# Performance work log

Measured on AMD Instinct MI355X. Metric: run time of the kernel, lower is better.

The kernel has to match this reference:

```python
import jax, jax.numpy as jnp
import numpy as np

B, T, D, H, HID = 1024, 128, 256, 512, 512
INITIAL_DT = 0.01
DT = 0.1  # uniform spacing of x_time -> n_tp == 1 every step (single Euler step)


def setup_inputs() -> dict:
    key = jax.random.key(0)
    ks = jax.random.split(key, 13)
    g = lambda k, shp, sc: (jax.random.normal(k, shp, dtype=jnp.float32) * sc)
    C = 2 * H + D  # GRU input: concat(h_mean, h_std, x)
    return {
        "x": jax.random.normal(ks[0], (B, T, D), dtype=jnp.float32),
        "x_time": jnp.arange(T, dtype=jnp.float32) * DT,
        # ODE func f(h): 2-layer tanh MLP
        "W1": g(ks[1], (H, HID), 1.0 / np.sqrt(H)),
        "b1": jnp.zeros((HID,), jnp.float32),
        "W2": g(ks[2], (HID, H), 1.0 / np.sqrt(HID)),
        "b2": jnp.zeros((H,), jnp.float32),
        # GRU unit (latent-ODE style): update gate, reset gate, new-state net
        "Wz": g(ks[3], (C, H), 1.0 / np.sqrt(C)),
        "bz": jnp.zeros((H,), jnp.float32),
        "Wr": g(ks[4], (C, H), 1.0 / np.sqrt(C)),
        "br": jnp.zeros((H,), jnp.float32),
        "Wn": g(ks[5], (C, 2 * H), 1.0 / np.sqrt(C)),
        "bn": jnp.zeros((2 * H,), jnp.float32),
    }


def reference(x, x_time, W1, b1, W2, b2, Wz, bz, Wr, br, Wn, bn):
    Bsz = x.shape[0]
    Hd = W1.shape[0]
    h0 = jnp.zeros((Bsz, Hd), x.dtype)
    std0 = jnp.zeros((Bsz, Hd), x.dtype)
    t0 = x_time[0] - INITIAL_DT

    def ode_f(h):  # dh/dt (autonomous MLP, as diffeq_solver ODE func)
        return jnp.tanh(h @ W1 + b1) @ W2 + b2

    def step(carry, inp):
        h, hstd, t_prev = carry
        xi, ti = inp
        dt = ti - t_prev
        # one Euler step of the ODE solver (n_tp<=1 for uniform x_time)
        h_ode = h + ode_f(h) * dt
        # GRU unit on (h_ode, hstd, xi)
        cat = jnp.concatenate([h_ode, hstd, xi], axis=-1)  # [B, 2H+D]
        z = jax.nn.sigmoid(cat @ Wz + bz)
        r = jax.nn.sigmoid(cat @ Wr + br)
        cat_r = jnp.concatenate([h_ode * r, hstd * r, xi], axis=-1)
        n_mean, n_std = jnp.split(cat_r @ Wn + bn, 2, axis=-1)
        n_std = jnp.abs(n_std)
        h_new = (1.0 - z) * n_mean + z * h_ode
        std_new = jnp.abs((1.0 - z) * n_std + z * hstd)
        return (h_new, std_new, ti), None

    xs = (jnp.swapaxes(x, 0, 1), x_time)  # [T,B,D], [T]
    (hT, stdT, _), _ = jax.lax.scan(step, (h0, std0, t0), xs)
    return hT, stdT
```

## Files before the change

kernel.cpp:

```cpp
#include <hip/hip_runtime.h>
#include <hip/hip_bf16.h>

#define B_SZ 1024
#define T_SZ 128
#define D_SZ 256
#define H_SZ 512
#define NBLK 256
#define NTHR 512
#define AUXS 0x1

typedef __attribute__((ext_vector_type(8))) short short8;
typedef __attribute__((ext_vector_type(4))) float f32x4;

__device__ inline f32x4 mfma16(short8 a, short8 b, f32x4 c) {
  return __builtin_amdgcn_mfma_f32_16x16x32_bf16(a, b, c, 0, 0, 0);
}

__device__ inline void st_bf16(__hip_bfloat16* p, float v) {
  union { __hip_bfloat16 b; unsigned short u; } cv;
  cv.b = __float2bfloat16(v);
  unsigned int vv = cv.u;
  asm volatile("global_store_short %0, %1, off" :: "v"(p), "v"(vv) : "memory");
}

template <int ROWS, int AUX>
__device__ __forceinline__ void stage512(const __hip_bfloat16* __restrict__ src,
                                         int strideElts, int row0, int k0,
                                         unsigned short* lds, int tid) {
  constexpr int CH = ROWS * 8;
#pragma unroll
  for (int it = 0; it * NTHR < CH; ++it) {
    int wbase = it * NTHR + ((tid >> 6) << 6);
    if (wbase < CH) {
      int chunk = it * NTHR + tid;
      int row = chunk >> 3, slot = chunk & 7;
      int ksrc = (slot ^ (row & 7)) << 3;
      const __hip_bfloat16* g = src + (size_t)(row0 + row) * strideElts + (k0 + ksrc);
      unsigned short* l = lds + (size_t)wbase * 8;
      __builtin_amdgcn_global_load_lds(
          (const __attribute__((address_space(1))) unsigned int*)g,
          (__attribute__((address_space(3))) unsigned int*)l, 16, 0, AUX);
    }
  }
}

__device__ __forceinline__ short8 ldfrag(const unsigned short* lds, int row, int slot) {
  int s = slot ^ (row & 7);
  return *(const short8*)(lds + row * 64 + s * 8);
}

template <int NT, int PB, typename SA, typename SB, typename CC>
__device__ __forceinline__ void gloop(int wv, SA sa, SB sb, CC cc) {
  sa(0, 0); sa(1, 1); sa(2, 2); sa(3, 3);
#pragma unroll 1
  for (int kt = 0; kt < NT; ++kt) {
    if (wv < 4) {
      if (kt == 0)           asm volatile("s_waitcnt vmcnt(3)" ::: "memory");
      else if (kt == 1)      asm volatile("s_waitcnt vmcnt(%0)" :: "i"(3 + PB) : "memory");
      else if (kt <= NT - 4) asm volatile("s_waitcnt vmcnt(%0)" :: "i"(3 + 2 * PB) : "memory");
      else if (kt == NT - 3) asm volatile("s_waitcnt vmcnt(%0)" :: "i"(2 + 2 * PB) : "memory");
      else if (kt == NT - 2) asm volatile("s_waitcnt vmcnt(%0)" :: "i"(1 + PB) : "memory");
      else                   asm volatile("s_waitcnt vmcnt(0)" ::: "memory");
    } else {
      if (kt <= NT - 3)      asm volatile("s_waitcnt vmcnt(%0)" :: "i"(2 * PB) : "memory");
      else if (kt == NT - 2) asm volatile("s_waitcnt vmcnt(%0)" :: "i"(PB) : "memory");
      else                   asm volatile("s_waitcnt vmcnt(0)" ::: "memory");
    }
    __builtin_amdgcn_s_barrier();
    __builtin_amdgcn_sched_barrier(0);
    if (kt + 3 < NT) sb(kt + 3, (kt + 3) & 3);
    if (kt + 4 < NT) sa(kt + 4, (kt + 4) % 5);
    cc(kt % 5, kt & 3);
  }
}

__device__ __forceinline__ void sbar_arrive(unsigned* scnt) {
  asm volatile("s_waitcnt vmcnt(0)" ::: "memory");
  __syncthreads();
  if (threadIdx.x == 0)
    __hip_atomic_fetch_add(scnt, 1u, __ATOMIC_RELAXED, __HIP_MEMORY_SCOPE_AGENT);
}
__device__ __forceinline__ void sbar_wait(unsigned* scnt, unsigned p) {
  if (threadIdx.x == 0) {
    while (__hip_atomic_load(scnt, __ATOMIC_RELAXED, __HIP_MEMORY_SCOPE_AGENT) < p * 8u)
      __builtin_amdgcn_s_sleep(1);
  }
  __syncthreads();
  __builtin_amdgcn_sched_barrier(0);
}

__global__ __launch_bounds__(512, 2) void k_fused(
    const float* __restrict__ xg, const float* __restrict__ xtime,
    const __hip_bfloat16* __restrict__ W1t, const float* __restrict__ b1,
    const __hip_bfloat16* __restrict__ W2t, const float* __restrict__ b2,
    const __hip_bfloat16* __restrict__ Wzrt, const float* __restrict__ bz,
    const float* __restrict__ br, const __hip_bfloat16* __restrict__ Wnt,
    const float* __restrict__ bn, float* __restrict__ hf, float* __restrict__ hstdf,
    __hip_bfloat16* __restrict__ hbf, __hip_bfloat16* __restrict__ Ubf,
    __hip_bfloat16* __restrict__ hodeb, __hip_bfloat16* __restrict__ hstdb,
    __hip_bfloat16* __restrict__ A4, __hip_bfloat16* __restrict__ xstep,
    unsigned* __restrict__ bar) {
  __shared__ __align__(16) unsigned short lA[5][32 * 64];
  __shared__ __align__(16) unsigned short lB[4][128 * 64];
  int tid = threadIdx.x, lane = tid & 63, wv = tid >> 6;
  int lr = lane & 15, lg = lane >> 4;
  int rh = wv >> 2, cq = wv & 3;
  int b = blockIdx.x;
  int xcd = b & 7;
  int j = b >> 3;
  int i = (xcd << 2) | (j >> 3);
  int s = j & 7;
  int m0 = i << 5;
  int nA = s << 6;
  unsigned* scnt = bar + i * 32;
  unsigned p = 0;
  int cl = (cq << 4) + lr;
  int col = nA + cl;
  int row0 = m0 + (rh << 4) + (lg << 2);
  float hreg[4] = {0.f, 0.f, 0.f, 0.f}, sreg[4] = {0.f, 0.f, 0.f, 0.f};
  float oreg[4], zreg[4];

  stage512<64, 0>(W1t, H_SZ, nA, 0, lB[0], tid);
  stage512<64, 0>(W1t, H_SZ, nA, 64, lB[1], tid);
  stage512<64, 0>(W1t, H_SZ, nA, 128, lB[2], tid);

#pragma unroll 1
  for (int t = 0; t < T_SZ; ++t) {
    {
      f32x4 acc = {};
      auto sa = [&](int kt, int bi) { stage512<32, AUXS>(hbf, H_SZ, m0, kt << 6, lA[bi], tid); };
      auto sb = [&](int kt, int bi) { stage512<64, 0>(W1t, H_SZ, nA, kt << 6, lB[bi], tid); };
      auto cc = [&](int ai, int bi) {
#pragma unroll
        for (int kk = 0; kk < 2; ++kk) {
          short8 a = ldfrag(lA[ai], (rh << 4) + lr, (kk << 2) + lg);
          short8 bb = ldfrag(lB[bi], cl, (kk << 2) + lg);
          acc = mfma16(a, bb, acc);
        }
      };
      gloop<8, 1>(wv, sa, sb, cc);
      float bi = b1[col];
#pragma unroll
      for (int r = 0; r < 4; ++r)
        st_bf16(&Ubf[(size_t)(row0 + r) * H_SZ + col], tanhf(acc[r] + bi));
    }
    sbar_arrive(scnt);
    stage512<64, 0>(W2t, H_SZ, nA, 0, lB[0], tid);
    stage512<64, 0>(W2t, H_SZ, nA, 64, lB[1], tid);
    stage512<64, 0>(W2t, H_SZ, nA, 128, lB[2], tid);
    sbar_wait(scnt, ++p);
    {
      f32x4 acc = {};
      auto sa = [&](int kt, int bi) { stage512<32, AUXS>(Ubf, H_SZ, m0, kt << 6, lA[bi], tid); };
      auto sb = [&](int kt, int bi) { stage512<64, 0>(W2t, H_SZ, nA, kt << 6, lB[bi], tid); };
      auto cc = [&](int ai, int bi) {
#pragma unroll
        for (int kk = 0; kk < 2; ++kk) {
          short8 a = ldfrag(lA[ai], (rh << 4) + lr, (kk << 2) + lg);
          short8 bb = ldfrag(lB[bi], cl, (kk << 2) + lg);
          acc = mfma16(a, bb, acc);
        }
      };
      gloop<8, 1>(wv, sa, sb, cc);
      float dtv = (t == 0) ? 0.01f : (xtime[t] - xtime[t - 1]);
      float bi = b2[col];
#pragma unroll
      for (int r = 0; r < 4; ++r) {
        float v = hreg[r] + dtv * (acc[r] + bi);
        oreg[r] = v;
        st_bf16(&hodeb[(size_t)(row0 + r) * H_SZ + col], v);
      }
      {
        int colx = (s << 5) + (tid & 31);
#pragma unroll
        for (int it2 = 0; it2 < 2; ++it2) {
          int row = m0 + (tid >> 5) + (it2 << 4);
          float xv = xg[((size_t)row * T_SZ + t) * D_SZ + colx];
          st_bf16(&xstep[(size_t)row * D_SZ + colx], xv);
        }
      }
    }
    sbar_arrive(scnt);
#pragma unroll
    for (int q = 0; q < 3; ++q) {
      stage512<64, 0>(Wzrt, 1280, nA, q << 6, lB[q], tid);
      stage512<64, 0>(Wzrt, 1280, 512 + nA, q << 6, lB[q] + 64 * 64, tid);
    }
    sbar_wait(scnt, ++p);
    {
      f32x4 acc0 = {}, acc1 = {};
      auto sa = [&](int kt, int bi) {
        int ke = kt << 6;
        if (ke < 512)       stage512<32, AUXS>(hodeb, H_SZ, m0, ke, lA[bi], tid);
        else if (ke < 1024) stage512<32, AUXS>(hstdb, H_SZ, m0, ke - 512, lA[bi], tid);
        else                stage512<32, AUXS>(xstep, D_SZ, m0, ke - 1024, lA[bi], tid);
      };
      auto sb = [&](int kt, int bi) {
        stage512<64, 0>(Wzrt, 1280, nA, kt << 6, lB[bi], tid);
        stage512<64, 0>(Wzrt, 1280, 512 + nA, kt << 6, lB[bi] + 64 * 64, tid);
      };
      auto cc = [&](int ai, int bi) {
#pragma unroll
        for (int kk = 0; kk < 2; ++kk) {
          short8 a = ldfrag(lA[ai], (rh << 4) + lr, (kk << 2) + lg);
          short8 b0 = ldfrag(lB[bi], cl, (kk << 2) + lg);
          short8 b1f = ldfrag(lB[bi], 64 + cl, (kk << 2) + lg);
          acc0 = mfma16(a, b0, acc0);
          acc1 = mfma16(a, b1f, acc1);
        }
      };
      gloop<20, 2>(wv, sa, sb, cc);
      float bz_ = bz[col], br_ = br[col];
#pragma unroll
      for (int r = 0; r < 4; ++r) {
        int row = row0 + r;
        zreg[r] = 1.f / (1.f + expf(-(acc0[r] + bz_)));
        float g = 1.f / (1.f + expf(-(acc1[r] + br_)));
        st_bf16(&A4[(size_t)row * 1024 + col], oreg[r] * g);
        st_bf16(&A4[(size_t)row * 1024 + 512 + col], sreg[r] * g);
      }
    }
    sbar_arrive(scnt);
#pragma unroll
    for (int q = 0; q < 3; ++q) {
      stage512<64, 0>(Wnt, 1280, nA, q << 6, lB[q], tid);
      stage512<64, 0>(Wnt, 1280, 512 + nA, q << 6, lB[q] + 64 * 64, tid);
    }
    sbar_wait(scnt, ++p);
    {
      f32x4 acc0 = {}, acc1 = {};
      auto sa = [&](int kt, int bi) {
        int ke = kt << 6;
        if (ke < 1024) stage512<32, AUXS>(A4, 1024, m0, ke, lA[bi], tid);
        else           stage512<32, AUXS>(xstep, D_SZ, m0, ke - 1024, lA[bi], tid);
      };
      auto sb = [&](int kt, int bi) {
        stage512<64, 0>(Wnt, 1280, nA, kt << 6, lB[bi], tid);
        stage512<64, 0>(Wnt, 1280, 512 + nA, kt << 6, lB[bi] + 64 * 64, tid);
      };
      auto cc = [&](int ai, int bi) {
#pragma unroll
        for (int kk = 0; kk < 2; ++kk) {
          short8 a = ldfrag(lA[ai], (rh << 4) + lr, (kk << 2) + lg);
          short8 b0 = ldfrag(lB[bi], cl, (kk << 2) + lg);
          short8 b1f = ldfrag(lB[bi], 64 + cl, (kk << 2) + lg);
          acc0 = mfma16(a, b0, acc0);
          acc1 = mfma16(a, b1f, acc1);
        }
      };
      gloop<20, 2>(wv, sa, sb, cc);
      float bm = bn[col], bs = bn[512 + col];
#pragma unroll
      for (int r = 0; r < 4; ++r) {
        int row = row0 + r;
        float z = zreg[r];
        float hn = (1.f - z) * (acc0[r] + bm) + z * oreg[r];
        hreg[r] = hn;
        st_bf16(&hbf[(size_t)row * H_SZ + col], hn);
        float ns = fabsf(acc1[r] + bs);
        float sn = fabsf((1.f - z) * ns + z * sreg[r]);
        sreg[r] = sn;
        st_bf16(&hstdb[(size_t)row * H_SZ + col], sn);
      }
    }
    sbar_arrive(scnt);
    stage512<64, 0>(W1t, H_SZ, nA, 0, lB[0], tid);
    stage512<64, 0>(W1t, H_SZ, nA, 64, lB[1], tid);
    stage512<64, 0>(W1t, H_SZ, nA, 128, lB[2], tid);
    sbar_wait(scnt, ++p);
  }
#pragma unroll
  for (int r = 0; r < 4; ++r) {
    int row = row0 + r;
    hf[(size_t)row * H_SZ + col] = hreg[r];
    hstdf[(size_t)row * H_SZ + col] = sreg[r];
  }
}

__global__ void k_wt(const float* __restrict__ W, __hip_bfloat16* __restrict__ Wt,
                     int K, int N, int ld) {
  size_t i = (size_t)blockIdx.x * 256 + threadIdx.x;
  if (i >= (size_t)K * N) return;
  int n = (int)(i / K), k = (int)(i % K);
  Wt[(size_t)n * ld + k] = __float2bfloat16(W[(size_t)k * N + n]);
}

extern "C" void kernel_launch(void* const* d_in, const int* in_sizes, int n_in,
                              void* d_out, int out_size, void* d_ws, size_t ws_size,
                              hipStream_t stream) {
  const float* x     = (const float*)d_in[0];
  const float* xtime = (const float*)d_in[1];
  const float* W1    = (const float*)d_in[2];
  const float* b1    = (const float*)d_in[3];
  const float* W2    = (const float*)d_in[4];
  const float* b2    = (const float*)d_in[5];
  const float* Wz    = (const float*)d_in[6];
  const float* bz    = (const float*)d_in[7];
  const float* Wr    = (const float*)d_in[8];
  const float* br    = (const float*)d_in[9];
  const float* Wn    = (const float*)d_in[10];
  const float* bn    = (const float*)d_in[11];

  char* p = (char*)d_ws;
  __hip_bfloat16* W1t   = (__hip_bfloat16*)(p + 0);
  __hip_bfloat16* W2t   = (__hip_bfloat16*)(p + 524288);
  __hip_bfloat16* Wzrt  = (__hip_bfloat16*)(p + 1048576);
  __hip_bfloat16* Wnt   = (__hip_bfloat16*)(p + 3670016);
  float*          hf    = (float*)(p + 6291456);
  float*          hstdf = (float*)(p + 8388608);
  __hip_bfloat16* hbf   = (__hip_bfloat16*)(p + 14680064);
  __hip_bfloat16* Ubf   = (__hip_bfloat16*)(p + 15728640);
  __hip_bfloat16* hodeb = (__hip_bfloat16*)(p + 16777216);
  __hip_bfloat16* hstdb = (__hip_bfloat16*)(p + 17825792);
  __hip_bfloat16* A4    = (__hip_bfloat16*)(p + 18874368);
  __hip_bfloat16* xstep = (__hip_bfloat16*)(p + 20971520);
  unsigned*       bar   = (unsigned*)(p + 21495808);

  hipMemsetAsync(hbf, 0, 1048576, stream);
  hipMemsetAsync(hstdb, 0, 1048576, stream);
  hipMemsetAsync(bar, 0, 8192, stream);

  k_wt<<<(512 * 512 + 255) / 256, 256, 0, stream>>>(W1, W1t, 512, 512, 512);
  k_wt<<<(512 * 512 + 255) / 256, 256, 0, stream>>>(W2, W2t, 512, 512, 512);
  k_wt<<<(1280 * 512 + 255) / 256, 256, 0, stream>>>(Wz, Wzrt, 1280, 512, 1280);
  k_wt<<<(1280 * 512 + 255) / 256, 256, 0, stream>>>(Wr, Wzrt + (size_t)512 * 1280, 1280, 512, 1280);
  k_wt<<<(1280 * 1024 + 255) / 256, 256, 0, stream>>>(Wn, Wnt, 1280, 1024, 1280);

  k_fused<<<NBLK, NTHR, 0, stream>>>(x, xtime, W1t, b1, W2t, b2, Wzrt, bz, br,
                                     Wnt, bn, hf, hstdf, hbf, Ubf,
                                     hodeb, hstdb, A4, xstep, bar);

  hipMemcpyAsync(d_out, hf, 2097152, hipMemcpyDeviceToDevice, stream);
  hipMemcpyAsync((char*)d_out + 2097152, hstdf, 2097152, hipMemcpyDeviceToDevice, stream);
}
```

Before: 4.996 ms.

## Load weight fragments directly from global and stage whole activation panels in LDS

```diff
diff --git a/kernel.cpp b/kernel.cpp
--- a/kernel.cpp
+++ b/kernel.cpp
@@ -23,24 +23,18 @@
   asm volatile("global_store_short %0, %1, off" :: "v"(p), "v"(vv) : "memory");
 }
 
-template <int ROWS, int AUX>
-__device__ __forceinline__ void stage512(const __hip_bfloat16* __restrict__ src,
-                                         int strideElts, int row0, int k0,
-                                         unsigned short* lds, int tid) {
-  constexpr int CH = ROWS * 8;
-#pragma unroll
-  for (int it = 0; it * NTHR < CH; ++it) {
-    int wbase = it * NTHR + ((tid >> 6) << 6);
-    if (wbase < CH) {
-      int chunk = it * NTHR + tid;
-      int row = chunk >> 3, slot = chunk & 7;
-      int ksrc = (slot ^ (row & 7)) << 3;
-      const __hip_bfloat16* g = src + (size_t)(row0 + row) * strideElts + (k0 + ksrc);
-      unsigned short* l = lds + (size_t)wbase * 8;
-      __builtin_amdgcn_global_load_lds(
-          (const __attribute__((address_space(1))) unsigned int*)g,
-          (__attribute__((address_space(3))) unsigned int*)l, 16, 0, AUX);
-    }
+template <int NT, typename F>
+__device__ __forceinline__ void stagePanel(unsigned short* pan, int tid, F src) {
+#pragma unroll
+  for (int it = 0; it * NTHR < NT * 256; ++it) {
+    int c = it * NTHR + tid;
+    int tile = c >> 8, row = (c >> 3) & 31, slot = c & 7;
+    int ksrc = (slot ^ (row & 7)) << 3;
+    const __hip_bfloat16* g = src(tile, row, ksrc);
+    unsigned short* l = pan + (size_t)(it * NTHR + ((tid >> 6) << 6)) * 8;
+    __builtin_amdgcn_global_load_lds(
+        (const __attribute__((address_space(1))) unsigned int*)g,
+        (__attribute__((address_space(3))) unsigned int*)l, 16, 0, AUXS);
   }
 }
 
@@ -49,44 +43,15 @@
   return *(const short8*)(lds + row * 64 + s * 8);
 }
 
-template <int NT, int PB, typename SA, typename SB, typename CC>
-__device__ __forceinline__ void gloop(int wv, SA sa, SB sb, CC cc) {
-  sa(0, 0); sa(1, 1); sa(2, 2); sa(3, 3);
-#pragma unroll 1
-  for (int kt = 0; kt < NT; ++kt) {
-    if (wv < 4) {
-      if (kt == 0)           asm volatile("s_waitcnt vmcnt(3)" ::: "memory");
-      else if (kt == 1)      asm volatile("s_waitcnt vmcnt(%0)" :: "i"(3 + PB) : "memory");
-      else if (kt <= NT - 4) asm volatile("s_waitcnt vmcnt(%0)" :: "i"(3 + 2 * PB) : "memory");
-      else if (kt == NT - 3) asm volatile("s_waitcnt vmcnt(%0)" :: "i"(2 + 2 * PB) : "memory");
-      else if (kt == NT - 2) asm volatile("s_waitcnt vmcnt(%0)" :: "i"(1 + PB) : "memory");
-      else                   asm volatile("s_waitcnt vmcnt(0)" ::: "memory");
-    } else {
-      if (kt <= NT - 3)      asm volatile("s_waitcnt vmcnt(%0)" :: "i"(2 * PB) : "memory");
-      else if (kt == NT - 2) asm volatile("s_waitcnt vmcnt(%0)" :: "i"(PB) : "memory");
-      else                   asm volatile("s_waitcnt vmcnt(0)" ::: "memory");
-    }
-    __builtin_amdgcn_s_barrier();
-    __builtin_amdgcn_sched_barrier(0);
-    if (kt + 3 < NT) sb(kt + 3, (kt + 3) & 3);
-    if (kt + 4 < NT) sa(kt + 4, (kt + 4) % 5);
-    cc(kt % 5, kt & 3);
-  }
-}
-
-__device__ __forceinline__ void sbar_arrive(unsigned* scnt) {
+__device__ __forceinline__ void sbar(unsigned* scnt, unsigned p) {
   asm volatile("s_waitcnt vmcnt(0)" ::: "memory");
   __syncthreads();
-  if (threadIdx.x == 0)
+  if (threadIdx.x == 0) {
     __hip_atomic_fetch_add(scnt, 1u, __ATOMIC_RELAXED, __HIP_MEMORY_SCOPE_AGENT);
-}
-__device__ __forceinline__ void sbar_wait(unsigned* scnt, unsigned p) {
-  if (threadIdx.x == 0) {
     while (__hip_atomic_load(scnt, __ATOMIC_RELAXED, __HIP_MEMORY_SCOPE_AGENT) < p * 8u)
       __builtin_amdgcn_s_sleep(1);
   }
   __syncthreads();
-  __builtin_amdgcn_sched_barrier(0);
 }
 
 __global__ __launch_bounds__(512, 2) void k_fused(
@@ -100,8 +65,7 @@
     __hip_bfloat16* __restrict__ hodeb, __hip_bfloat16* __restrict__ hstdb,
     __hip_bfloat16* __restrict__ A4, __hip_bfloat16* __restrict__ xstep,
     unsigned* __restrict__ bar) {
-  __shared__ __align__(16) unsigned short lA[5][32 * 64];
-  __shared__ __align__(16) unsigned short lB[4][128 * 64];
+  __shared__ __align__(16) unsigned short pan[20 * 32 * 64];
   int tid = threadIdx.x, lane = tid & 63, wv = tid >> 6;
   int lr = lane & 15, lg = lane >> 4;
   int rh = wv >> 2, cq = wv & 3;
@@ -120,48 +84,52 @@
   float hreg[4] = {0.f, 0.f, 0.f, 0.f}, sreg[4] = {0.f, 0.f, 0.f, 0.f};
   float oreg[4], zreg[4];
 
-  stage512<64, 0>(W1t, H_SZ, nA, 0, lB[0], tid);
-  stage512<64, 0>(W1t, H_SZ, nA, 64, lB[1], tid);
-  stage512<64, 0>(W1t, H_SZ, nA, 128, lB[2], tid);
+  const __hip_bfloat16* w1p = W1t + (size_t)(nA + cl) * H_SZ + (lg << 3);
+  const __hip_bfloat16* w2p = W2t + (size_t)(nA + cl) * H_SZ + (lg << 3);
+  const __hip_bfloat16* wzp = Wzrt + (size_t)(nA + cl) * 1280 + (lg << 3);
+  const __hip_bfloat16* wrp = Wzrt + (size_t)(512 + nA + cl) * 1280 + (lg << 3);
+  const __hip_bfloat16* wmp = Wnt + (size_t)(nA + cl) * 1280 + (lg << 3);
+  const __hip_bfloat16* wsp = Wnt + (size_t)(512 + nA + cl) * 1280 + (lg << 3);
 
 #pragma unroll 1
   for (int t = 0; t < T_SZ; ++t) {
-    {
+    sbar(scnt, ++p);
+    {
+      stagePanel<8>(pan, tid, [&](int tile, int row, int ks) {
+        return hbf + (size_t)(m0 + row) * H_SZ + (tile << 6) + ks;
+      });
+      asm volatile("s_waitcnt vmcnt(0)" ::: "memory");
+      __syncthreads();
       f32x4 acc = {};
-      auto sa = [&](int kt, int bi) { stage512<32, AUXS>(hbf, H_SZ, m0, kt << 6, lA[bi], tid); };
-      auto sb = [&](int kt, int bi) { stage512<64, 0>(W1t, H_SZ, nA, kt << 6, lB[bi], tid); };
-      auto cc = [&](int ai, int bi) {
-#pragma unroll
-        for (int kk = 0; kk < 2; ++kk) {
-          short8 a = ldfrag(lA[ai], (rh << 4) + lr, (kk << 2) + lg);
-          short8 bb = ldfrag(lB[bi], cl, (kk << 2) + lg);
+#pragma unroll
+      for (int kt = 0; kt < 8; ++kt)
+#pragma unroll
+        for (int kk = 0; kk < 2; ++kk) {
+          short8 a = ldfrag(pan + (kt << 11), (rh << 4) + lr, (kk << 2) + lg);
+          short8 bb = *(const short8*)(w1p + (kt << 6) + (kk << 5));
           acc = mfma16(a, bb, acc);
         }
-      };
-      gloop<8, 1>(wv, sa, sb, cc);
       float bi = b1[col];
 #pragma unroll
       for (int r = 0; r < 4; ++r)
         st_bf16(&Ubf[(size_t)(row0 + r) * H_SZ + col], tanhf(acc[r] + bi));
     }
-    sbar_arrive(scnt);
-    stage512<64, 0>(W2t, H_SZ, nA, 0, lB[0], tid);
-    stage512<64, 0>(W2t, H_SZ, nA, 64, lB[1], tid);
-    stage512<64, 0>(W2t, H_SZ, nA, 128, lB[2], tid);
-    sbar_wait(scnt, ++p);
-    {
+    sbar(scnt, ++p);
+    {
+      stagePanel<8>(pan, tid, [&](int tile, int row, int ks) {
+        return Ubf + (size_t)(m0 + row) * H_SZ + (tile << 6) + ks;
+      });
+      asm volatile("s_waitcnt vmcnt(0)" ::: "memory");
+      __syncthreads();
       f32x4 acc = {};
-      auto sa = [&](int kt, int bi) { stage512<32, AUXS>(Ubf, H_SZ, m0, kt << 6, lA[bi], tid); };
-      auto sb = [&](int kt, int bi) { stage512<64, 0>(W2t, H_SZ, nA, kt << 6, lB[bi], tid); };
-      auto cc = [&](int ai, int bi) {
-#pragma unroll
-        for (int kk = 0; kk < 2; ++kk) {
-          short8 a = ldfrag(lA[ai], (rh << 4) + lr, (kk << 2) + lg);
-          short8 bb = ldfrag(lB[bi], cl, (kk << 2) + lg);
+#pragma unroll
+      for (int kt = 0; kt < 8; ++kt)
+#pragma unroll
+        for (int kk = 0; kk < 2; ++kk) {
+          short8 a = ldfrag(pan + (kt << 11), (rh << 4) + lr, (kk << 2) + lg);
+          short8 bb = *(const short8*)(w2p + (kt << 6) + (kk << 5));
           acc = mfma16(a, bb, acc);
         }
-      };
-      gloop<8, 1>(wv, sa, sb, cc);
       float dtv = (t == 0) ? 0.01f : (xtime[t] - xtime[t - 1]);
       float bi = b2[col];
 #pragma unroll
@@ -180,36 +148,27 @@
         }
       }
     }
-    sbar_arrive(scnt);
-#pragma unroll
-    for (int q = 0; q < 3; ++q) {
-      stage512<64, 0>(Wzrt, 1280, nA, q << 6, lB[q], tid);
-      stage512<64, 0>(Wzrt, 1280, 512 + nA, q << 6, lB[q] + 64 * 64, tid);
-    }
-    sbar_wait(scnt, ++p);
-    {
+    sbar(scnt, ++p);
+    {
+      stagePanel<20>(pan, tid, [&](int tile, int row, int ks) -> const __hip_bfloat16* {
+        int ke = tile << 6;
+        if (ke < 512)  return hodeb + (size_t)(m0 + row) * H_SZ + ke + ks;
+        if (ke < 1024) return hstdb + (size_t)(m0 + row) * H_SZ + (ke - 512) + ks;
+        return xstep + (size_t)(m0 + row) * D_SZ + (ke - 1024) + ks;
+      });
+      asm volatile("s_waitcnt vmcnt(0)" ::: "memory");
+      __syncthreads();
       f32x4 acc0 = {}, acc1 = {};
-      auto sa = [&](int kt, int bi) {
-        int ke = kt << 6;
-        if (ke < 512)       stage512<32, AUXS>(hodeb, H_SZ, m0, ke, lA[bi], tid);
-        else if (ke < 1024) stage512<32, AUXS>(hstdb, H_SZ, m0, ke - 512, lA[bi], tid);
-        else                stage512<32, AUXS>(xstep, D_SZ, m0, ke - 1024, lA[bi], tid);
-      };
-      auto sb = [&](int kt, int bi) {
-        stage512<64, 0>(Wzrt, 1280, nA, kt << 6, lB[bi], tid);
-        stage512<64, 0>(Wzrt, 1280, 512 + nA, kt << 6, lB[bi] + 64 * 64, tid);
-      };
-      auto cc = [&](int ai, int bi) {
-#pragma unroll
-        for (int kk = 0; kk < 2; ++kk) {
-          short8 a = ldfrag(lA[ai], (rh << 4) + lr, (kk << 2) + lg);
-          short8 b0 = ldfrag(lB[bi], cl, (kk << 2) + lg);
-          short8 b1f = ldfrag(lB[bi], 64 + cl, (kk << 2) + lg);
+#pragma unroll
+      for (int kt = 0; kt < 20; ++kt)
+#pragma unroll
+        for (int kk = 0; kk < 2; ++kk) {
+          short8 a = ldfrag(pan + (kt << 11), (rh << 4) + lr, (kk << 2) + lg);
+          short8 b0 = *(const short8*)(wzp + (kt << 6) + (kk << 5));
+          short8 b1f = *(const short8*)(wrp + (kt << 6) + (kk << 5));
           acc0 = mfma16(a, b0, acc0);
           acc1 = mfma16(a, b1f, acc1);
         }
-      };
-      gloop<20, 2>(wv, sa, sb, cc);
       float bz_ = bz[col], br_ = br[col];
 #pragma unroll
       for (int r = 0; r < 4; ++r) {
@@ -220,35 +179,26 @@
         st_bf16(&A4[(size_t)row * 1024 + 512 + col], sreg[r] * g);
       }
     }
-    sbar_arrive(scnt);
-#pragma unroll
-    for (int q = 0; q < 3; ++q) {
-      stage512<64, 0>(Wnt, 1280, nA, q << 6, lB[q], tid);
-      stage512<64, 0>(Wnt, 1280, 512 + nA, q << 6, lB[q] + 64 * 64, tid);
-    }
-    sbar_wait(scnt, ++p);
-    {
+    sbar(scnt, ++p);
+    {
+      stagePanel<20>(pan, tid, [&](int tile, int row, int ks) -> const __hip_bfloat16* {
+        int ke = tile << 6;
+        if (ke < 1024) return A4 + (size_t)(m0 + row) * 1024 + ke + ks;
+        return xstep + (size_t)(m0 + row) * D_SZ + (ke - 1024) + ks;
+      });
+      asm volatile("s_waitcnt vmcnt(0)" ::: "memory");
+      __syncthreads();
       f32x4 acc0 = {}, acc1 = {};
-      auto sa = [&](int kt, int bi) {
-        int ke = kt << 6;
-        if (ke < 1024) stage512<32, AUXS>(A4, 1024, m0, ke, lA[bi], tid);
-        else           stage512<32, AUXS>(xstep, D_SZ, m0, ke - 1024, lA[bi], tid);
-      };
-      auto sb = [&](int kt, int bi) {
-        stage512<64, 0>(Wnt, 1280, nA, kt << 6, lB[bi], tid);
-        stage512<64, 0>(Wnt, 1280, 512 + nA, kt << 6, lB[bi] + 64 * 64, tid);
-      };
-      auto cc = [&](int ai, int bi) {
-#pragma unroll
-        for (int kk = 0; kk < 2; ++kk) {
-          short8 a = ldfrag(lA[ai], (rh << 4) + lr, (kk << 2) + lg);
-          short8 b0 = ldfrag(lB[bi], cl, (kk << 2) + lg);
-          short8 b1f = ldfrag(lB[bi], 64 + cl, (kk << 2) + lg);
+#pragma unroll
+      for (int kt = 0; kt < 20; ++kt)
+#pragma unroll
+        for (int kk = 0; kk < 2; ++kk) {
+          short8 a = ldfrag(pan + (kt << 11), (rh << 4) + lr, (kk << 2) + lg);
+          short8 b0 = *(const short8*)(wmp + (kt << 6) + (kk << 5));
+          short8 b1f = *(const short8*)(wsp + (kt << 6) + (kk << 5));
           acc0 = mfma16(a, b0, acc0);
           acc1 = mfma16(a, b1f, acc1);
         }
-      };
-      gloop<20, 2>(wv, sa, sb, cc);
       float bm = bn[col], bs = bn[512 + col];
 #pragma unroll
       for (int r = 0; r < 4; ++r) {
@@ -263,11 +213,6 @@
         st_bf16(&hstdb[(size_t)row * H_SZ + col], sn);
       }
     }
-    sbar_arrive(scnt);
-    stage512<64, 0>(W1t, H_SZ, nA, 0, lB[0], tid);
-    stage512<64, 0>(W1t, H_SZ, nA, 64, lB[1], tid);
-    stage512<64, 0>(W1t, H_SZ, nA, 128, lB[2], tid);
-    sbar_wait(scnt, ++p);
   }
 #pragma unroll
   for (int r = 0; r < 4; ++r) {
```

Result: slower. 6.483 ms (+29.8%).
